# Kernel optimization log

Hardware: AMD Instinct MI355X
Metric: run time of the kernel (lower is better)

## Reference

```python
import jax, jax.numpy as jnp
import numpy as np

B, T1, T2, D, O = 8, 64, 128, 512, 512

def setup_inputs() -> dict:
    key = jax.random.key(0)
    k1, k2, k3 = jax.random.split(key, 3)
    X = jax.random.normal(k1, (B, T1, T2, D), dtype=jnp.float32)
    W = jax.random.normal(k2, (D, O), dtype=jnp.float32) * (1.0 / np.sqrt(D))
    b = jax.random.normal(k3, (O,), dtype=jnp.float32) * 0.01
    return {"X": X, "W": W, "b": b}

def reference(X, W, b):
    # Original serializes this via nested K.rnn scans over time1/time2, but the
    # math is a single per-position dense + bias + tanh activation.
    # btsd,do->btso
    return jnp.tanh(jnp.einsum("btsd,do->btso", X, W) + b)
```

## Files before the change

### kernel.cpp

```cpp
#include <hip/hip_runtime.h>
#include <stdint.h>


typedef short bf16x8 __attribute__((ext_vector_type(8)));
typedef float f32x16 __attribute__((ext_vector_type(16)));

#define KTOT 512
#define NTOT 512
#define WT_BYTES   524288ull
#define WS_NEEDED  WT_BYTES

__device__ __forceinline__ uint32_t pk2(float a, float b) {
  uint16_t lo = __builtin_bit_cast(uint16_t, (__bf16)a);
  uint16_t hi = __builtin_bit_cast(uint16_t, (__bf16)b);
  return (uint32_t)lo | ((uint32_t)hi << 16);
}

__device__ __forceinline__ float fast_tanh(float z) {
  float t = __builtin_amdgcn_exp2f(z * 2.8853900817779268f);
  return 1.0f - 2.0f * __builtin_amdgcn_rcpf(t + 1.0f);
}

#define MFMA(A, B, C) __builtin_amdgcn_mfma_f32_32x32x16_bf16(A, B, C, 0, 0, 0)

__global__ __launch_bounds__(256)
void cvtW_kernel(const float* __restrict__ W, uint8_t* __restrict__ Wt) {
  const int c    = blockIdx.x * 256 + threadIdx.x;
  const int lane = c & 63;
  const int nf   = (c >> 6) & 3;
  const int k16  = (c >> 8) & 31;
  const int wq   = c >> 13;
  const int col  = wq * 128 + nf * 32 + (lane & 31);
  const int kb   = k16 * 16 + (lane >> 5) * 8;
  float e[8];
#pragma unroll
  for (int i = 0; i < 8; ++i) e[i] = W[(size_t)(kb + i) * NTOT + col];
  *(uint4*)(Wt + (size_t)c * 16) =
      make_uint4(pk2(e[0], e[1]), pk2(e[2], e[3]),
                 pk2(e[4], e[5]), pk2(e[6], e[7]));
}

__global__ __launch_bounds__(256, 2)
void hotdd_fused(const float* __restrict__ X, const uint8_t* __restrict__ Wt,
                 const float* __restrict__ Bv, float* __restrict__ Y) {
  __shared__ uint8_t Ab[65536];

  const int bm   = blockIdx.x;
  const int tid  = threadIdx.x;
  const int lane = tid & 63;
  const int wv   = tid >> 6;
  const int lo5  = lane & 31;
  const int hi1  = lane >> 5;

#define SEP() asm volatile("" ::: "memory")
#define VM(N) asm volatile("s_waitcnt vmcnt(" #N ")" ::: "memory")

  const float* Xs = X + (size_t)bm * (64 * KTOT);
  const int chunkT = (tid >> 1) & 63;
  const int halfT  = tid & 1;
  const int rbT    = tid >> 7;

  float4 p00, p01, p02, p03, p10, p11, p12, p13;

#define LOADP(R0, R1, R2, R3, B) do {                                         \
    const float* q_ = Xs + (size_t)(B) * 4096 + tid * 4;                      \
    R0 = *(const float4*)q_;          R1 = *(const float4*)(q_ + 1024);       \
    R2 = *(const float4*)(q_ + 2048); R3 = *(const float4*)(q_ + 3072);       \
    SEP();                                                                    \
  } while (0)

#define CVTP1(R, J) do {                                                      \
    const int row_ = 2 * (J) + rbT;                                           \
    *(uint2*)(Ab + row_ * 1024 + ((chunkT ^ row_) << 4) + halfT * 8) =        \
        make_uint2(pk2(R.x, R.y), pk2(R.z, R.w));                             \
  } while (0)
#define CVTP(R0, R1, R2, R3, B) do {                                          \
    CVTP1(R0, 4 * (B));     CVTP1(R1, 4 * (B) + 1);                           \
    CVTP1(R2, 4 * (B) + 2); CVTP1(R3, 4 * (B) + 3);  SEP();                   \
  } while (0)

  LOADP(p00, p01, p02, p03, 0);
  LOADP(p10, p11, p12, p13, 1);
  VM(4); CVTP(p00, p01, p02, p03, 0); LOADP(p00, p01, p02, p03, 2);
  VM(4); CVTP(p10, p11, p12, p13, 1); LOADP(p10, p11, p12, p13, 3);
  VM(4); CVTP(p00, p01, p02, p03, 2); LOADP(p00, p01, p02, p03, 4);
  VM(4); CVTP(p10, p11, p12, p13, 3); LOADP(p10, p11, p12, p13, 5);
  VM(4); CVTP(p00, p01, p02, p03, 4); LOADP(p00, p01, p02, p03, 6);
  VM(4); CVTP(p10, p11, p12, p13, 5); LOADP(p10, p11, p12, p13, 7);
  VM(4); CVTP(p00, p01, p02, p03, 6);
  VM(0); CVTP(p10, p11, p12, p13, 7);

  const uint8_t* pBw = Wt + (size_t)wv * 131072 + lane * 16;
  bf16x8 e0, e1, e2, e3, o0, o1, o2, o3, f0, f1, f2, f3;

#define LOADB(S0, S1, S2, S3, T) do {                                         \
    const uint8_t* q_ = pBw + (size_t)(T) * 4096;                             \
    S0 = *(const bf16x8*)q_;            S1 = *(const bf16x8*)(q_ + 1024);     \
    S2 = *(const bf16x8*)(q_ + 2048);   S3 = *(const bf16x8*)(q_ + 3072);     \
    SEP();                                                                    \
  } while (0)

  LOADB(e0, e1, e2, e3, 0);
  LOADB(o0, o1, o2, o3, 1);
  __syncthreads();

  f32x16 c00 = {}, c01 = {}, c02 = {}, c03 = {};
  f32x16 c10 = {}, c11 = {}, c12 = {}, c13 = {};
  const int ardA = lo5 << 10;
  const int ardB = (lo5 + 32) << 10;

#define COMP(T, S0, S1, S2, S3) do {                                          \
    const int cb_ = (((((T) << 1) | hi1)) ^ lo5) << 4;                        \
    bf16x8 fa0 = *(const bf16x8*)(Ab + ardA + cb_);                           \
    bf16x8 fa1 = *(const bf16x8*)(Ab + ardB + (cb_ ^ 512));                   \
    c00 = MFMA(fa0, S0, c00);  c01 = MFMA(fa0, S1, c01);                      \
    c02 = MFMA(fa0, S2, c02);  c03 = MFMA(fa0, S3, c03);                      \
    c10 = MFMA(fa1, S0, c10);  c11 = MFMA(fa1, S1, c11);                      \
    c12 = MFMA(fa1, S2, c12);  c13 = MFMA(fa1, S3, c13);                      \
  } while (0)

#pragma unroll 1
  for (int t = 0; t < 30; t += 3) {
    LOADB(f0, f1, f2, f3, t + 2);  VM(8);  COMP(t,     e0, e1, e2, e3);
    LOADB(e0, e1, e2, e3, t + 3);  VM(8);  COMP(t + 1, o0, o1, o2, o3);
    LOADB(o0, o1, o2, o3, t + 4);  VM(8);  COMP(t + 2, f0, f1, f2, f3);
  }
  VM(4);  COMP(30, e0, e1, e2, e3);
  VM(0);  COMP(31, o0, o1, o2, o3);

  const int colb = wv * 128 + lo5;
  const float bv0 = Bv[colb];
  const float bv1 = Bv[colb + 32];
  const float bv2 = Bv[colb + 64];
  const float bv3 = Bv[colb + 96];
  const size_t rowbase = (size_t)bm * 64 + (hi1 << 2);

#define EPI(ACC, MI, NF, BV) do {                                             \
    _Pragma("unroll")                                                         \
    for (int r = 0; r < 16; ++r) {                                            \
      const size_t row_ = rowbase + (MI) * 32 + (r & 3) + ((r >> 2) << 3);    \
      Y[row_ * NTOT + colb + (NF) * 32] = fast_tanh((ACC)[r] + (BV));         \
    }                                                                         \
  } while (0)

  EPI(c00, 0, 0, bv0);  EPI(c01, 0, 1, bv1);
  EPI(c02, 0, 2, bv2);  EPI(c03, 0, 3, bv3);
  EPI(c10, 1, 0, bv0);  EPI(c11, 1, 1, bv1);
  EPI(c12, 1, 2, bv2);  EPI(c13, 1, 3, bv3);
}

struct Regs {
  float4 a0,a1,a2,a3,a4,a5,a6,a7;
  float4 u0,u1,u2,u3;
  float4 v0,v1,v2,v3;
};

__global__ __launch_bounds__(256, 2)
void hotdd_fallback(const float* __restrict__ X, const float* __restrict__ W,
                    const float* __restrict__ Bv, float* __restrict__ Y) {
  __shared__ char Ab[128 * 64 * 2];
  __shared__ char Bb[128 * 64 * 2];
  const int d  = blockIdx.x;
  const int bm = ((d >> 5) << 3) | (d & 7);
  const int bn = (d >> 3) & 3;
  const int tid  = threadIdx.x;
  const int lane = tid & 63;
  const int wv   = tid >> 6;
  const int wr   = (wv >> 1) * 64;
  const int wc   = (wv & 1) * 64;
  const int lo5  = lane & 31;
  const int hi1  = lane >> 5;
  const int rs   = lo5 & 7;
  const int am   = tid >> 1;
  const int ah   = tid & 1;
  const int amz  = am & 7;
  const int abase = am * 128;
  const float* Ag = X + (size_t)(bm * 128 + am) * KTOT + ah * 32;
  const int kp = lo5;
  const int ng = wv * 32 + hi1 * 16;
  const float* Bg = W + (size_t)(2 * kp) * NTOT + bn * 128 + ng;

#define LOADR(R, K0) do {                                                     \
    const float* ap_ = Ag + (K0);                                             \
    R.a0 = *(const float4*)(ap_ +  0); R.a1 = *(const float4*)(ap_ +  4);     \
    R.a2 = *(const float4*)(ap_ +  8); R.a3 = *(const float4*)(ap_ + 12);     \
    R.a4 = *(const float4*)(ap_ + 16); R.a5 = *(const float4*)(ap_ + 20);     \
    R.a6 = *(const float4*)(ap_ + 24); R.a7 = *(const float4*)(ap_ + 28);     \
    const float* bp_ = Bg + (size_t)(K0) * NTOT;                              \
    R.u0 = *(const float4*)(bp_ +  0); R.u1 = *(const float4*)(bp_ +  4);     \
    R.u2 = *(const float4*)(bp_ +  8); R.u3 = *(const float4*)(bp_ + 12);     \
    R.v0 = *(const float4*)(bp_ + NTOT +  0); R.v1 = *(const float4*)(bp_ + NTOT +  4); \
    R.v2 = *(const float4*)(bp_ + NTOT +  8); R.v3 = *(const float4*)(bp_ + NTOT + 12); \
  } while (0)

#define ASTF(R, J, P, Q)                                                      \
    *(uint4*)(Ab + abase + (((((ah << 2) + (J)) ^ amz)) << 4)) =              \
      make_uint4(pk2(R.P.x, R.P.y), pk2(R.P.z, R.P.w),                        \
                 pk2(R.Q.x, R.Q.y), pk2(R.Q.z, R.Q.w));
#define BSTF(R, I, UV, C)                                                     \
    *(uint32_t*)(Bb + (ng + (I)) * 128 + ((kp << 2) ^ (((I) & 7) << 4))) =    \
      pk2(R.u##UV.C, R.v##UV.C);

#define STORERF(R) do {                                                       \
    ASTF(R, 0, a0, a1) ASTF(R, 1, a2, a3) ASTF(R, 2, a4, a5) ASTF(R, 3, a6, a7)\
    BSTF(R, 0, 0, x) BSTF(R, 1, 0, y) BSTF(R, 2, 0, z) BSTF(R, 3, 0, w)       \
    BSTF(R, 4, 1, x) BSTF(R, 5, 1, y) BSTF(R, 6, 1, z) BSTF(R, 7, 1, w)       \
    BSTF(R, 8, 2, x) BSTF(R, 9, 2, y) BSTF(R,10, 2, z) BSTF(R,11, 2, w)       \
    BSTF(R,12, 3, x) BSTF(R,13, 3, y) BSTF(R,14, 3, z) BSTF(R,15, 3, w)       \
  } while (0)

  f32x16 acc00 = {}, acc01 = {}, acc10 = {}, acc11 = {};
  const char* Ard0 = Ab + (wr + lo5) * 128;
  const char* Ard1 = Ard0 + 32 * 128;
  const char* Brd0 = Bb + (wc + lo5) * 128;
  const char* Brd1 = Brd0 + 32 * 128;

#define MFMA_PHASE_F() do {                                                   \
    _Pragma("unroll")                                                         \
    for (int kk = 0; kk < 4; ++kk) {                                          \
      const int sb = ((((kk << 1) | hi1) ^ rs) << 4);                         \
      bf16x8 fa0 = *(const bf16x8*)(Ard0 + sb);                               \
      bf16x8 fa1 = *(const bf16x8*)(Ard1 + sb);                               \
      bf16x8 fb0 = *(const bf16x8*)(Brd0 + sb);                               \
      bf16x8 fb1 = *(const bf16x8*)(Brd1 + sb);                               \
      acc00 = MFMA(fa0, fb0, acc00);  acc01 = MFMA(fa0, fb1, acc01);          \
      acc10 = MFMA(fa1, fb0, acc10);  acc11 = MFMA(fa1, fb1, acc11);          \
    }                                                                         \
  } while (0)

  Regs r0, r1;
  LOADR(r0, 0);
#pragma unroll 1
  for (int s = 0; s < 8; s += 2) {
    STORERF(r0);
    __syncthreads();
    LOADR(r1, (s + 1) * 64);
    MFMA_PHASE_F();
    __syncthreads();
    STORERF(r1);
    __syncthreads();
    if (s + 2 < 8) LOADR(r0, (s + 2) * 64);
    MFMA_PHASE_F();
    __syncthreads();
  }

  const int gn0 = bn * 128 + wc + lo5;
  const int gn1 = gn0 + 32;
  const float bv0 = Bv[gn0];
  const float bv1 = Bv[gn1];

#define EPIF(ACC, MI, GN, BVAL) do {                                          \
    _Pragma("unroll")                                                         \
    for (int r = 0; r < 16; ++r) {                                            \
      const int mloc = wr + (MI) * 32 + (hi1 << 2) + ((r >> 2) << 3) + (r & 3);\
      Y[(size_t)(bm * 128 + mloc) * NTOT + (GN)] = fast_tanh((ACC)[r] + (BVAL));\
    }                                                                         \
  } while (0)

  EPIF(acc00, 0, gn0, bv0);
  EPIF(acc01, 0, gn1, bv1);
  EPIF(acc10, 1, gn0, bv0);
  EPIF(acc11, 1, gn1, bv1);
}

extern "C" void kernel_launch(void* const* d_in, const int* in_sizes, int n_in,
                              void* d_out, int out_size, void* d_ws, size_t ws_size,
                              hipStream_t stream) {
  (void)in_sizes; (void)n_in; (void)out_size;
  const float* X = (const float*)d_in[0];
  const float* W = (const float*)d_in[1];
  const float* b = (const float*)d_in[2];
  float* Y = (float*)d_out;
  if (ws_size >= WS_NEEDED) {
    uint8_t* Wt = (uint8_t*)d_ws;
    hipLaunchKernelGGL(cvtW_kernel, dim3(128),  dim3(256), 0, stream, W, Wt);
    hipLaunchKernelGGL(hotdd_fused, dim3(1024), dim3(256), 0, stream, X, Wt, b, Y);
  } else {
    hipLaunchKernelGGL(hotdd_fallback, dim3(2048), dim3(256), 0, stream, X, W, b, Y);
  }
}
```

Before: 72.03 us.

## Make fused GEMM persistent with double-buffered X tiles overlapped with MFMA

The fused kernel now launches 256 blocks that each handle four 64-row tiles in sequence, instead of 1024 blocks with one tile each. LDS doubles to 128KB to double-buffer the bf16 A tile, so the next tile's X load and conversion run inside the current tile's MFMA loop, and the B pipeline deepens to four register sets. This hides the X load latency behind compute, at the cost of one block per CU and higher register pressure. The epilogue stores are not overlapped, and 256 blocks may not fill all CUs evenly.

New measurement: 70.52 us. 1.02x faster.

```diff
diff --git a/kernel.cpp b/kernel.cpp
--- a/kernel.cpp
+++ b/kernel.cpp
@@ -40,10 +40,10 @@
                  pk2(e[4], e[5]), pk2(e[6], e[7]));
 }
 
-__global__ __launch_bounds__(256, 2)
+__global__ __launch_bounds__(256, 1)
 void hotdd_fused(const float* __restrict__ X, const uint8_t* __restrict__ Wt,
                  const float* __restrict__ Bv, float* __restrict__ Y) {
-  __shared__ uint8_t Ab[65536];
+  __shared__ uint8_t Ab[131072];
 
   const int bm   = blockIdx.x;
   const int tid  = threadIdx.x;
@@ -51,102 +51,163 @@
   const int wv   = tid >> 6;
   const int lo5  = lane & 31;
   const int hi1  = lane >> 5;
-
-#define SEP() asm volatile("" ::: "memory")
-#define VM(N) asm volatile("s_waitcnt vmcnt(" #N ")" ::: "memory")
-
-  const float* Xs = X + (size_t)bm * (64 * KTOT);
   const int chunkT = (tid >> 1) & 63;
   const int halfT  = tid & 1;
   const int rbT    = tid >> 7;
 
+#define SEP() asm volatile("" ::: "memory")
+#define VM(N) asm volatile("s_waitcnt vmcnt(" #N ")" ::: "memory")
+
   float4 p00, p01, p02, p03, p10, p11, p12, p13;
 
-#define LOADP(R0, R1, R2, R3, B) do {                                         \
-    const float* q_ = Xs + (size_t)(B) * 4096 + tid * 4;                      \
+#define PLOAD(R0, R1, R2, R3, BASE, B) do {                                   \
+    const float* q_ = (BASE) + (size_t)(B) * 4096 + tid * 4;                  \
     R0 = *(const float4*)q_;          R1 = *(const float4*)(q_ + 1024);       \
     R2 = *(const float4*)(q_ + 2048); R3 = *(const float4*)(q_ + 3072);       \
     SEP();                                                                    \
   } while (0)
 
-#define CVTP1(R, J) do {                                                      \
-    const int row_ = 2 * (J) + rbT;                                           \
-    *(uint2*)(Ab + row_ * 1024 + ((chunkT ^ row_) << 4) + halfT * 8) =        \
-        make_uint2(pk2(R.x, R.y), pk2(R.z, R.w));                             \
-  } while (0)
-#define CVTP(R0, R1, R2, R3, B) do {                                          \
-    CVTP1(R0, 4 * (B));     CVTP1(R1, 4 * (B) + 1);                           \
-    CVTP1(R2, 4 * (B) + 2); CVTP1(R3, 4 * (B) + 3);  SEP();                   \
-  } while (0)
-
-  LOADP(p00, p01, p02, p03, 0);
-  LOADP(p10, p11, p12, p13, 1);
-  VM(4); CVTP(p00, p01, p02, p03, 0); LOADP(p00, p01, p02, p03, 2);
-  VM(4); CVTP(p10, p11, p12, p13, 1); LOADP(p10, p11, p12, p13, 3);
-  VM(4); CVTP(p00, p01, p02, p03, 2); LOADP(p00, p01, p02, p03, 4);
-  VM(4); CVTP(p10, p11, p12, p13, 3); LOADP(p10, p11, p12, p13, 5);
-  VM(4); CVTP(p00, p01, p02, p03, 4); LOADP(p00, p01, p02, p03, 6);
-  VM(4); CVTP(p10, p11, p12, p13, 5); LOADP(p10, p11, p12, p13, 7);
-  VM(4); CVTP(p00, p01, p02, p03, 6);
-  VM(0); CVTP(p10, p11, p12, p13, 7);
+#define PCVT1(R, ROW, DST)                                                    \
+    *(uint2*)(Ab + (DST) + (ROW) * 1024 + (((chunkT) ^ (ROW)) << 4)           \
+              + halfT * 8) = make_uint2(pk2(R.x, R.y), pk2(R.z, R.w));
+#define PCVT(R0, R1, R2, R3, B, DST) do {                                     \
+    const int rb_ = 8 * (B) + rbT;                                            \
+    PCVT1(R0, rb_,     DST)  PCVT1(R1, rb_ + 2, DST)                          \
+    PCVT1(R2, rb_ + 4, DST)  PCVT1(R3, rb_ + 6, DST)  SEP();                  \
+  } while (0)
+
+  const float* Xs0 = X + (size_t)bm * (64 * KTOT);
+  PLOAD(p00, p01, p02, p03, Xs0, 0);
+  PLOAD(p10, p11, p12, p13, Xs0, 1);
+  VM(4); PCVT(p00, p01, p02, p03, 0, 0); PLOAD(p00, p01, p02, p03, Xs0, 2);
+  VM(4); PCVT(p10, p11, p12, p13, 1, 0); PLOAD(p10, p11, p12, p13, Xs0, 3);
+  VM(4); PCVT(p00, p01, p02, p03, 2, 0); PLOAD(p00, p01, p02, p03, Xs0, 4);
+  VM(4); PCVT(p10, p11, p12, p13, 3, 0); PLOAD(p10, p11, p12, p13, Xs0, 5);
+  VM(4); PCVT(p00, p01, p02, p03, 4, 0); PLOAD(p00, p01, p02, p03, Xs0, 6);
+  VM(4); PCVT(p10, p11, p12, p13, 5, 0); PLOAD(p10, p11, p12, p13, Xs0, 7);
+  VM(4); PCVT(p00, p01, p02, p03, 6, 0);
+  VM(0); PCVT(p10, p11, p12, p13, 7, 0);
 
   const uint8_t* pBw = Wt + (size_t)wv * 131072 + lane * 16;
-  bf16x8 e0, e1, e2, e3, o0, o1, o2, o3, f0, f1, f2, f3;
-
-#define LOADB(S0, S1, S2, S3, T) do {                                         \
+  bf16x8 bA0,bA1,bA2,bA3, bB0,bB1,bB2,bB3, bC0,bC1,bC2,bC3, bD0,bD1,bD2,bD3;
+
+#define LODB(S0, S1, S2, S3, T) do {                                          \
     const uint8_t* q_ = pBw + (size_t)(T) * 4096;                             \
     S0 = *(const bf16x8*)q_;            S1 = *(const bf16x8*)(q_ + 1024);     \
     S2 = *(const bf16x8*)(q_ + 2048);   S3 = *(const bf16x8*)(q_ + 3072);     \
     SEP();                                                                    \
   } while (0)
 
-  LOADB(e0, e1, e2, e3, 0);
-  LOADB(o0, o1, o2, o3, 1);
+  LODB(bA0,bA1,bA2,bA3, 0);
+  LODB(bB0,bB1,bB2,bB3, 1);
+  PLOAD(p00, p01, p02, p03, X + (size_t)(bm + 256) * (64 * KTOT), 0);
   __syncthreads();
 
   f32x16 c00 = {}, c01 = {}, c02 = {}, c03 = {};
   f32x16 c10 = {}, c11 = {}, c12 = {}, c13 = {};
-  const int ardA = lo5 << 10;
-  const int ardB = (lo5 + 32) << 10;
-
-#define COMP(T, S0, S1, S2, S3) do {                                          \
+
+#define COMP(T, S0, S1, S2, S3, CUR) do {                                     \
     const int cb_ = (((((T) << 1) | hi1)) ^ lo5) << 4;                        \
-    bf16x8 fa0 = *(const bf16x8*)(Ab + ardA + cb_);                           \
-    bf16x8 fa1 = *(const bf16x8*)(Ab + ardB + (cb_ ^ 512));                   \
+    bf16x8 fa0 = *(const bf16x8*)(Ab + (CUR) + (lo5 << 10) + cb_);            \
+    bf16x8 fa1 = *(const bf16x8*)(Ab + (CUR) + ((lo5 + 32) << 10)             \
+                                  + (cb_ ^ 512));                             \
     c00 = MFMA(fa0, S0, c00);  c01 = MFMA(fa0, S1, c01);                      \
     c02 = MFMA(fa0, S2, c02);  c03 = MFMA(fa0, S3, c03);                      \
     c10 = MFMA(fa1, S0, c10);  c11 = MFMA(fa1, S1, c11);                      \
     c12 = MFMA(fa1, S2, c12);  c13 = MFMA(fa1, S3, c13);                      \
   } while (0)
-
-#pragma unroll 1
-  for (int t = 0; t < 30; t += 3) {
-    LOADB(f0, f1, f2, f3, t + 2);  VM(8);  COMP(t,     e0, e1, e2, e3);
-    LOADB(e0, e1, e2, e3, t + 3);  VM(8);  COMP(t + 1, o0, o1, o2, o3);
-    LOADB(o0, o1, o2, o3, t + 4);  VM(8);  COMP(t + 2, f0, f1, f2, f3);
-  }
-  VM(4);  COMP(30, e0, e1, e2, e3);
-  VM(0);  COMP(31, o0, o1, o2, o3);
 
   const int colb = wv * 128 + lo5;
   const float bv0 = Bv[colb];
   const float bv1 = Bv[colb + 32];
   const float bv2 = Bv[colb + 64];
   const float bv3 = Bv[colb + 96];
-  const size_t rowbase = (size_t)bm * 64 + (hi1 << 2);
-
-#define EPI(ACC, MI, NF, BV) do {                                             \
+
+#define EPI1(ACC, MI, NF, BV, RB) do {                                        \
     _Pragma("unroll")                                                         \
     for (int r = 0; r < 16; ++r) {                                            \
-      const size_t row_ = rowbase + (MI) * 32 + (r & 3) + ((r >> 2) << 3);    \
+      const size_t row_ = (RB) + (MI) * 32 + (r & 3) + ((r >> 2) << 3);       \
       Y[row_ * NTOT + colb + (NF) * 32] = fast_tanh((ACC)[r] + (BV));         \
     }                                                                         \
   } while (0)
 
-  EPI(c00, 0, 0, bv0);  EPI(c01, 0, 1, bv1);
-  EPI(c02, 0, 2, bv2);  EPI(c03, 0, 3, bv3);
-  EPI(c10, 1, 0, bv0);  EPI(c11, 1, 1, bv1);
-  EPI(c12, 1, 2, bv2);  EPI(c13, 1, 3, bv3);
+  int curOff = 0;
+
+#pragma unroll 1
+  for (int s = 0; s < 4; ++s) {
+    const int nxtOff = curOff ^ 65536;
+    const float* pXn = X + (size_t)(bm + (((s + 1) & 3) << 8)) * (64 * KTOT);
+
+    if (s < 3) {
+#pragma unroll 1
+      for (int g = 0; g < 7; ++g) {
+        const int t_ = g << 2;
+        LODB(bC0,bC1,bC2,bC3, t_ + 2);
+        VM(8);
+        PCVT(p00, p01, p02, p03, g, nxtOff);
+        COMP(t_,     bA0,bA1,bA2,bA3, curOff);
+        PLOAD(p00, p01, p02, p03, pXn, g + 1);
+        LODB(bD0,bD1,bD2,bD3, t_ + 3);
+        VM(12);
+        COMP(t_ + 1, bB0,bB1,bB2,bB3, curOff);
+        LODB(bA0,bA1,bA2,bA3, t_ + 4);
+        VM(12);
+        COMP(t_ + 2, bC0,bC1,bC2,bC3, curOff);
+        LODB(bB0,bB1,bB2,bB3, t_ + 5);
+        VM(8);
+        COMP(t_ + 3, bD0,bD1,bD2,bD3, curOff);
+      }
+      LODB(bC0,bC1,bC2,bC3, 30);
+      VM(8);  PCVT(p00, p01, p02, p03, 7, nxtOff);
+      COMP(28, bA0,bA1,bA2,bA3, curOff);
+      LODB(bD0,bD1,bD2,bD3, 31);
+      VM(8);  COMP(29, bB0,bB1,bB2,bB3, curOff);
+      VM(4);  COMP(30, bC0,bC1,bC2,bC3, curOff);
+      VM(0);  COMP(31, bD0,bD1,bD2,bD3, curOff);
+    } else {
+#pragma unroll 1
+      for (int g = 0; g < 7; ++g) {
+        const int t_ = g << 2;
+        LODB(bC0,bC1,bC2,bC3, t_ + 2);  VM(8);
+        COMP(t_,     bA0,bA1,bA2,bA3, curOff);
+        LODB(bD0,bD1,bD2,bD3, t_ + 3);  VM(8);
+        COMP(t_ + 1, bB0,bB1,bB2,bB3, curOff);
+        LODB(bA0,bA1,bA2,bA3, t_ + 4);  VM(8);
+        COMP(t_ + 2, bC0,bC1,bC2,bC3, curOff);
+        LODB(bB0,bB1,bB2,bB3, t_ + 5);  VM(8);
+        COMP(t_ + 3, bD0,bD1,bD2,bD3, curOff);
+      }
+      LODB(bC0,bC1,bC2,bC3, 30);
+      VM(8);  COMP(28, bA0,bA1,bA2,bA3, curOff);
+      LODB(bD0,bD1,bD2,bD3, 31);
+      VM(8);  COMP(29, bB0,bB1,bB2,bB3, curOff);
+      VM(4);  COMP(30, bC0,bC1,bC2,bC3, curOff);
+      VM(0);  COMP(31, bD0,bD1,bD2,bD3, curOff);
+    }
+
+    __syncthreads();
+
+    if (s < 2) {
+      const float* pXn2 = X + (size_t)(bm + ((s + 2) << 8)) * (64 * KTOT);
+      PLOAD(p00, p01, p02, p03, pXn2, 0);
+    }
+
+    {
+      const size_t rb = (size_t)(bm + (s << 8)) * 64 + (hi1 << 2);
+      EPI1(c00, 0, 0, bv0, rb);  EPI1(c01, 0, 1, bv1, rb);
+      EPI1(c02, 0, 2, bv2, rb);  EPI1(c03, 0, 3, bv3, rb);
+      EPI1(c10, 1, 0, bv0, rb);  EPI1(c11, 1, 1, bv1, rb);
+      EPI1(c12, 1, 2, bv2, rb);  EPI1(c13, 1, 3, bv3, rb);
+      c00 = (f32x16){}; c01 = (f32x16){}; c02 = (f32x16){}; c03 = (f32x16){};
+      c10 = (f32x16){}; c11 = (f32x16){}; c12 = (f32x16){}; c13 = (f32x16){};
+    }
+
+    if (s < 3) {
+      LODB(bA0,bA1,bA2,bA3, 0);
+      LODB(bB0,bB1,bB2,bB3, 1);
+    }
+    curOff = nxtOff;
+  }
 }
 
 struct Regs {
@@ -273,8 +334,8 @@
   float* Y = (float*)d_out;
   if (ws_size >= WS_NEEDED) {
     uint8_t* Wt = (uint8_t*)d_ws;
-    hipLaunchKernelGGL(cvtW_kernel, dim3(128),  dim3(256), 0, stream, W, Wt);
-    hipLaunchKernelGGL(hotdd_fused, dim3(1024), dim3(256), 0, stream, X, Wt, b, Y);
+    hipLaunchKernelGGL(cvtW_kernel, dim3(128), dim3(256), 0, stream, W, Wt);
+    hipLaunchKernelGGL(hotdd_fused, dim3(256), dim3(256), 0, stream, X, Wt, b, Y);
   } else {
     hipLaunchKernelGGL(hotdd_fallback, dim3(2048), dim3(256), 0, stream, X, W, b, Y);
   }
```
